# Performance work log

Hardware: AMD Instinct MI355X
Metric: run time of the kernel (lower is better)

The kernel has to match this reference:

```python
import jax, jax.numpy as jnp
import numpy as np

# Model constants (from source: model_dim=1024, head_dim=128, num_heads=8)
L = 8          # num layers (reduced from 16 for tractable reference memory)
T = 2048       # packed tokens, B == 1 (varlen)
DIM = 1024
NH = 8
NKV = 4        # GQA kv heads
HD = 128
KVD = NKV * HD
BLOCK = 128
WS = 3
WIN = WS * BLOCK           # sliding-window size for 'S' layers
ATTN_SCALE = 0.12
PATTERN = 'SSSL'
GATE_CH = 32
EPS = 1.1920929e-07        # torch F.rms_norm default eps = finfo(fp32).eps


def rms_norm(x):
    return x * jax.lax.rsqrt(jnp.mean(x * x, axis=-1, keepdims=True) + EPS)


def apply_rotary(x, cos, sin):
    # x: [T, H, HD]; cos/sin: [T, 1, HD//2]
    d = x.shape[-1] // 2
    x1, x2 = x[..., :d], x[..., d:]
    return jnp.concatenate([x1 * cos + x2 * sin, -x1 * sin + x2 * cos], axis=-1)


def has_ve(layer_idx, n_layer):
    return layer_idx % 2 == (n_layer - 1) % 2


def setup_inputs() -> dict:
    key = jax.random.key(0)
    ks = jax.random.split(key, 9)
    x = jax.random.normal(ks[0], (1, T, DIM), jnp.float32)
    ve = jax.random.normal(ks[1], (L, T, KVD), jnp.float32)
    s = DIM ** -0.5
    Wq = jax.random.normal(ks[2], (L, DIM, NH * HD), jnp.float32) * s
    Wk = jax.random.normal(ks[3], (L, DIM, KVD), jnp.float32) * s
    Wv = jax.random.normal(ks[4], (L, DIM, KVD), jnp.float32) * s
    Wo = jax.random.normal(ks[5], (L, NH * HD, DIM), jnp.float32) * (NH * HD) ** -0.5
    Wgate = jax.random.normal(ks[6], (L, GATE_CH, NKV), jnp.float32) * GATE_CH ** -0.5
    Wfc = jax.random.normal(ks[7], (L, DIM, 4 * DIM), jnp.float32) * s
    Wproj = jax.random.normal(ks[8], (L, 4 * DIM, DIM), jnp.float32) * (4 * DIM) ** -0.5
    # RoPE tables (absolute positions of the packed batch, as in the source)
    inv_freq = 1.0 / (10000.0 ** (jnp.arange(HD // 2, dtype=jnp.float32) / (HD // 2)))
    ang = jnp.arange(T, dtype=jnp.float32)[:, None] * inv_freq[None, :]
    cos = jnp.cos(ang)[:, None, :]
    sin = jnp.sin(ang)[:, None, :]
    # cu_seqlens: 4 packed documents of 512 tokens
    seqlens = jnp.array([0, 512, 1024, 1536, 2048], dtype=jnp.int32)
    return dict(x=x, ve=ve, Wq=Wq, Wk=Wk, Wv=Wv, Wo=Wo, Wgate=Wgate,
                Wfc=Wfc, Wproj=Wproj, cos=cos, sin=sin, seqlens=seqlens)


def reference(x, ve, Wq, Wk, Wv, Wo, Wgate, Wfc, Wproj, cos, sin, seqlens):
    h = x[0]  # [T, DIM], B == 1 (varlen packing)
    pos = jnp.arange(T)
    doc = jnp.searchsorted(seqlens, pos, side='right') - 1
    diff = pos[:, None] - pos[None, :]
    base = (diff >= 0) & (doc[:, None] == doc[None, :])   # causal within doc
    mask_S = base & (diff <= WIN)                         # sliding window
    neg = jnp.float32(-1e30)
    rep = NH // NKV
    for l in range(L):
        xn = rms_norm(h)
        q = (xn @ Wq[l]).reshape(T, NH, HD)
        k = (xn @ Wk[l]).reshape(T, NKV, HD)
        v = (xn @ Wv[l]).reshape(T, NKV, HD)
        if has_ve(l, L):
            gate = 2.0 * jax.nn.sigmoid(xn[:, :GATE_CH] @ Wgate[l])  # [T, NKV]
            v = v + gate[:, :, None] * ve[l].reshape(T, NKV, HD)
        q = rms_norm(apply_rotary(q, cos, sin))
        k = rms_norm(apply_rotary(k, cos, sin))
        k = jnp.repeat(k, rep, axis=1)   # GQA -> full heads
        v2 = jnp.repeat(v, rep, axis=1)
        scores = jnp.einsum('thd,shd->hts', q, k) * ATTN_SCALE  # [NH, T, T]
        mask = mask_S if PATTERN[l % len(PATTERN)] == 'S' else base
        scores = jnp.where(mask[None], scores, neg)
        p = jax.nn.softmax(scores, axis=-1)
        y = jnp.einsum('hts,shd->thd', p, v2).reshape(T, NH * HD)
        h = h + y @ Wo[l]
        m = jnp.square(jax.nn.relu(rms_norm(h) @ Wfc[l]))  # relu(x)^2 MLP
        h = h + m @ Wproj[l]
    return h[None]
```

## Files before the change

kernel.cpp:

```cpp
#include <hip/hip_runtime.h>
#include <hip/hip_bf16.h>
#include <cstdint>
#include <cstddef>

#define TT     2048
#define DMODEL 1024
#define NHQ    8
#define HD     128
#define KVD    512
#define WIN    384
#define EPSF   1.1920929e-07f
#define SCALE  0.12f

typedef __attribute__((ext_vector_type(8))) short bf16x8;
typedef __attribute__((ext_vector_type(4))) float f32x4;

#define WAITV(N)  asm volatile("s_waitcnt vmcnt(" #N ")" ::: "memory")

__device__ __forceinline__ float b2f(unsigned short u) {
    unsigned int i = ((unsigned int)u) << 16; float f; __builtin_memcpy(&f, &i, 4); return f;
}
__device__ __forceinline__ unsigned short f2b(float f) {
    unsigned int i; __builtin_memcpy(&i, &f, 4);
    unsigned int r = (i + 0x7fffu + ((i >> 16) & 1u)) >> 16;
    return (unsigned short)r;
}

__device__ __forceinline__ void gl_lds16(const unsigned short* g, unsigned short* l) {
    __builtin_amdgcn_global_load_lds(
        (const __attribute__((address_space(1))) unsigned int*)g,
        (__attribute__((address_space(3))) unsigned int*)l, 16, 0, 0);
}

__global__ __launch_bounds__(256)
void convT_k(const float* __restrict__ Wq, const float* __restrict__ Wk,
             const float* __restrict__ Wv, const float* __restrict__ Wo,
             const float* __restrict__ Wfc, const float* __restrict__ Wproj,
             unsigned short* __restrict__ Bqkv, unsigned short* __restrict__ Bo,
             unsigned short* __restrict__ Bfc, unsigned short* __restrict__ Bproj)
{
    __shared__ float lt[64][65];
    const int bid = blockIdx.x, tid = threadIdx.x, l = blockIdx.y;

    const float* W; unsigned short* Wt; int K, N, t, nbase;
    if (bid < 256)        { W = Wq    + (size_t)l * 1024 * 1024; Wt = Bqkv  + (size_t)l * 2048 * 1024; K = 1024; N = 1024; t = bid;        nbase = 0;    }
    else if (bid < 384)   { W = Wk    + (size_t)l * 1024 * 512;  Wt = Bqkv  + (size_t)l * 2048 * 1024; K = 1024; N = 512;  t = bid - 256;  nbase = 1024; }
    else if (bid < 512)   { W = Wv    + (size_t)l * 1024 * 512;  Wt = Bqkv  + (size_t)l * 2048 * 1024; K = 1024; N = 512;  t = bid - 384;  nbase = 1536; }
    else if (bid < 768)   { W = Wo    + (size_t)l * 1024 * 1024; Wt = Bo    + (size_t)l * 1024 * 1024; K = 1024; N = 1024; t = bid - 512;  nbase = 0;    }
    else if (bid < 1792)  { W = Wfc   + (size_t)l * 1024 * 4096; Wt = Bfc   + (size_t)l * 4096 * 1024; K = 1024; N = 4096; t = bid - 768;  nbase = 0;    }
    else                  { W = Wproj + (size_t)l * 4096 * 1024; Wt = Bproj + (size_t)l * 1024 * 4096; K = 4096; N = 1024; t = bid - 1792; nbase = 0;    }

    const int ktiles = K >> 6;
    const int k0 = (t % ktiles) * 64, n0 = (t / ktiles) * 64;

    #pragma unroll
    for (int i = 0; i < 4; ++i) {
        int k = (tid >> 4) + i * 16;
        int col4 = (tid & 15) * 4;
        float4 v = *(const float4*)(W + (size_t)(k0 + k) * N + n0 + col4);
        lt[col4 + 0][k] = v.x;
        lt[col4 + 1][k] = v.y;
        lt[col4 + 2][k] = v.z;
        lt[col4 + 3][k] = v.w;
    }
    __syncthreads();
    #pragma unroll
    for (int i = 0; i < 2; ++i) {
        int idx = tid + i * 256;
        int n = idx >> 3, kc = (idx & 7) * 8;
        unsigned short o[8];
        #pragma unroll
        for (int j = 0; j < 8; ++j) o[j] = f2b(lt[n][kc + j]);
        *(uint4*)(Wt + (size_t)(nbase + n0 + n) * K + k0 + kc) = *(const uint4*)o;
    }
}

template<int EPI>
__global__ __launch_bounds__(256, 2)
void gemm4(const unsigned short* __restrict__ A, const unsigned short* __restrict__ Bt,
           unsigned short* __restrict__ Cp, int K, int ksplit, int Ntot)
{
    __shared__ unsigned short As[2 * 128 * 64];
    __shared__ unsigned short Bs[2 * 128 * 64];
    const int BUF = 128 * 64;
    const int tid = threadIdx.x, lane = tid & 63, wv = tid >> 6;

    const int gx = gridDim.x;
    const int nwg = gx * gridDim.y;
    const int ihw = blockIdx.y * gx + blockIdx.x;
    const int q = nwg >> 3, r = nwg & 7;
    const int xcd = ihw & 7, pos = ihw >> 3;
    const int lg = (xcd < r) ? xcd * (q + 1) + pos
                             : r * (q + 1) + (xcd - r) * q + pos;
    const int m0 = (lg % gx) * 128, n0 = (lg / gx) * 128;

    const int kbeg = blockIdx.z * ksplit;
    const int NT = ksplit >> 6;

    const int wr = (wv >> 1) * 64, wc = (wv & 1) * 64;
    const int l15 = lane & 15, g = lane >> 4;
    const int srow = lane >> 3;
    const int sxor = (((lane & 7) ^ srow) << 3);

    const unsigned short* gA0 = A  + (size_t)(m0 + wv * 32 + srow) * K + sxor;
    const unsigned short* gB0 = Bt + (size_t)(n0 + wv * 32 + srow) * K + sxor;

    auto stage = [&](int t) {
        const int b = t & 1;
        const size_t k = (size_t)kbeg + ((size_t)t << 6);
        unsigned short* la = As + b * BUF + (wv * 32) * 64;
        unsigned short* lb = Bs + b * BUF + (wv * 32) * 64;
        #pragma unroll
        for (int c = 0; c < 4; ++c) {
            gl_lds16(gA0 + (size_t)(c * 8) * K + k, la + c * 8 * 64);
            gl_lds16(gB0 + (size_t)(c * 8) * K + k, lb + c * 8 * 64);
        }
    };

    f32x4 acc[4][4] = {};

    stage(0);
    for (int t = 0; t < NT; ++t) {
        if (t + 1 < NT) { stage(t + 1); WAITV(8); }
        else            { WAITV(0); }
        __builtin_amdgcn_s_barrier();

        const unsigned short* Ac = As + (t & 1) * BUF;
        const unsigned short* Bc = Bs + (t & 1) * BUF;
        bf16x8 af[4][2], bfv[4][2];
        #pragma unroll
        for (int mi = 0; mi < 4; ++mi) {
            const int row = wr + mi * 16 + l15, x = row & 7;
            #pragma unroll
            for (int kk = 0; kk < 2; ++kk)
                af[mi][kk] = *(const bf16x8*)(Ac + row * 64 + (((kk * 4 + g) ^ x) << 3));
        }
        #pragma unroll
        for (int ni = 0; ni < 4; ++ni) {
            const int row = wc + ni * 16 + l15, x = row & 7;
            #pragma unroll
            for (int kk = 0; kk < 2; ++kk)
                bfv[ni][kk] = *(const bf16x8*)(Bc + row * 64 + (((kk * 4 + g) ^ x) << 3));
        }
        __builtin_amdgcn_s_setprio(1);
        #pragma unroll
        for (int kk = 0; kk < 2; ++kk)
            #pragma unroll
            for (int mi = 0; mi < 4; ++mi)
                #pragma unroll
                for (int ni = 0; ni < 4; ++ni)
                    acc[mi][ni] = __builtin_amdgcn_mfma_f32_16x16x32_bf16(af[mi][kk], bfv[ni][kk], acc[mi][ni], 0, 0, 0);
        __builtin_amdgcn_s_setprio(0);
        __builtin_amdgcn_s_barrier();
    }

    const int lr4 = (lane >> 4) * 4;
    unsigned short* Cz = Cp + (size_t)blockIdx.z * TT * Ntot;
    #pragma unroll
    for (int mi = 0; mi < 4; ++mi)
        #pragma unroll
        for (int ni = 0; ni < 4; ++ni)
            #pragma unroll
            for (int r2 = 0; r2 < 4; ++r2) {
                int row = m0 + wr + mi * 16 + lr4 + r2;
                int col = n0 + wc + ni * 16 + l15;
                size_t idx = (size_t)row * Ntot + col;
                float v = acc[mi][ni][r2];
                if (EPI == 0) Cz[idx] = f2b(v);
                else {
                    float z = v > 0.f ? v * v : 0.f;
                    Cz[idx] = f2b(z);
                }
            }
}

__global__ __launch_bounds__(256)
void rmsnormF_k(float* __restrict__ h, const unsigned short* __restrict__ part, int nz,
                unsigned short* __restrict__ xn)
{
    const int t = blockIdx.x, tid = threadIdx.x;
    const size_t idx = (size_t)t * (DMODEL / 4) + tid;
    float4 v = ((const float4*)h)[idx];
    for (int z = 0; z < nz; ++z) {
        ushort4 p = ((const ushort4*)part)[idx + (size_t)z * (TT * DMODEL / 4)];
        v.x += b2f(p.x); v.y += b2f(p.y); v.z += b2f(p.z); v.w += b2f(p.w);
    }
    if (nz > 0) ((float4*)h)[idx] = v;

    float ss = v.x*v.x + v.y*v.y + v.z*v.z + v.w*v.w;
    #pragma unroll
    for (int m = 1; m < 64; m <<= 1) ss += __shfl_xor(ss, m);
    __shared__ float red[4];
    if ((tid & 63) == 0) red[tid >> 6] = ss;
    __syncthreads();
    float tot = red[0] + red[1] + red[2] + red[3];
    float rs = rsqrtf(tot * (1.f / DMODEL) + EPSF);
    unsigned short o[4] = { f2b(v.x*rs), f2b(v.y*rs), f2b(v.z*rs), f2b(v.w*rs) };
    *(ushort4*)(xn + (size_t)t * DMODEL + tid * 4) = *(const ushort4*)o;
}

__global__ __launch_bounds__(256)
void reduce_add_k(float* __restrict__ h, const unsigned short* __restrict__ part, int nz)
{
    const int i = blockIdx.x * 256 + threadIdx.x;
    float4 hv = ((float4*)h)[i];
    for (int z = 0; z < nz; ++z) {
        ushort4 p = ((const ushort4*)part)[i + (size_t)z * (TT * DMODEL / 4)];
        hv.x += b2f(p.x); hv.y += b2f(p.y); hv.z += b2f(p.z); hv.w += b2f(p.w);
    }
    ((float4*)h)[i] = hv;
}

__global__ __launch_bounds__(256)
void post_qkv_k(const unsigned short* __restrict__ qkv, const unsigned short* __restrict__ xn,
                const float* __restrict__ cosb, const float* __restrict__ sinb,
                const float* __restrict__ Wgate, const float* __restrict__ vel, int hasve,
                unsigned short* __restrict__ qn, unsigned short* __restrict__ kn,
                unsigned short* __restrict__ vrow)
{
    const size_t S2 = (size_t)TT * 2048;
    const int t = blockIdx.x, tid = threadIdx.x;
    __shared__ float cs[64], sn[64], gate[4];
    if (tid < 64) { cs[tid] = cosb[t * 64 + tid]; sn[tid] = sinb[t * 64 + tid]; }
    if (hasve && tid >= 64 && tid < 68) {
        int g = tid - 64; float a = 0.f;
        for (int c = 0; c < 32; ++c) a += b2f(xn[(size_t)t * DMODEL + c]) * Wgate[c * 4 + g];
        gate[g] = 2.f / (1.f + __expf(-a));
    }
    __syncthreads();
    if (tid < 96) {
        const int hid = tid >> 3, sub = tid & 7;
        const unsigned short* src; unsigned short* dst;
        if (hid < 8) { src = qkv + (size_t)t * 2048 + hid * 128;              dst = qn + (size_t)t * 1024 + hid * 128; }
        else         { src = qkv + (size_t)t * 2048 + 1024 + (hid - 8) * 128; dst = kn + (size_t)t * 512 + (hid - 8) * 128; }
        float o1[8], o2[8], ssum = 0.f;
        #pragma unroll
        for (int j = 0; j < 8; ++j) {
            int jj = sub * 8 + j;
            float x1 = b2f(src[jj])      + b2f(src[jj + S2]);
            float x2 = b2f(src[jj + 64]) + b2f(src[jj + 64 + S2]);
            float c = cs[jj], s = sn[jj];
            o1[j] = x1 * c + x2 * s;
            o2[j] = -x1 * s + x2 * c;
            ssum += o1[j]*o1[j] + o2[j]*o2[j];
        }
        ssum += __shfl_xor(ssum, 1); ssum += __shfl_xor(ssum, 2); ssum += __shfl_xor(ssum, 4);
        float rs = rsqrtf(ssum * (1.f / HD) + EPSF);
        #pragma unroll
        for (int j = 0; j < 8; ++j) {
            int jj = sub * 8 + j;
            dst[jj]      = f2b(o1[j] * rs);
            dst[jj + 64] = f2b(o2[j] * rs);
        }
    }
    {
        int d0 = tid * 2;
        #pragma unroll
        for (int j = 0; j < 2; ++j) {
            int d = d0 + j;
            size_t off = (size_t)t * 2048 + 1536 + d;
            float vv = b2f(qkv[off]) + b2f(qkv[off + S2]);
            if (hasve) vv += gate[d >> 7] * vel[(size_t)t * KVD + d];
            vrow[(size_t)t * KVD + d] = f2b(vv);
        }
    }
}

__global__ __launch_bounds__(256)
void vtrans_k(const unsigned short* __restrict__ vrow, unsigned short* __restrict__ vt)
{
    __shared__ unsigned short lt[64][72];
    const int t0 = blockIdx.x * 64, c0 = blockIdx.y * 64, tid = threadIdx.x;
    #pragma unroll
    for (int i = 0; i < 2; ++i) {
        int r = (tid >> 3) + i * 32;
        int c = (tid & 7) * 8;
        bf16x8 v = *(const bf16x8*)(vrow + (size_t)(t0 + r) * KVD + c0 + c);
        #pragma unroll
        for (int j = 0; j < 8; ++j) lt[c + j][r] = ((unsigned short*)&v)[j];
    }
    __syncthreads();
    #pragma unroll
    for (int i = 0; i < 2; ++i) {
        int r = (tid >> 3) + i * 32;
        int c = (tid & 7) * 8;
        *(bf16x8*)(vt + (size_t)(c0 + r) * TT + t0 + c) = *(const bf16x8*)(&lt[r][c]);
    }
}

__global__ __launch_bounds__(256)
void attn_k(const unsigned short* __restrict__ qn, const unsigned short* __restrict__ kn,
            const unsigned short* __restrict__ vt, unsigned short* __restrict__ y,
            const int* __restrict__ seqlens, int isS)
{
    __shared__ float Ot[4][16][132];
    const int tid = threadIdx.x, w = tid >> 6, lane = tid & 63;
    const int h = blockIdx.y, hkv = h >> 1;
    const int qr = (blockIdx.x * 4 + w) * 16;
    const int s1 = seqlens[1], s2 = seqlens[2], s3 = seqlens[3];
    const int l15 = lane & 15, g = lane >> 4;

    bf16x8 qf[4];
    #pragma unroll
    for (int kk = 0; kk < 4; ++kk)
        qf[kk] = *(const bf16x8*)(qn + (size_t)(qr + l15) * 1024 + h * HD + kk * 32 + g * 8);

    const int row = qr + l15;
    const int drow = (row >= s1) + (row >= s2) + (row >= s3);

    int dq = (qr >= s1) + (qr >= s2) + (qr >= s3);
    int dstart = dq == 0 ? 0 : (dq == 1 ? s1 : (dq == 2 ? s2 : s3));
    int smin = dstart;
    if (isS) { int wlo = qr - WIN; if (wlo > smin) smin = wlo; }
    if (smin < 0) smin = 0;
    const int smax = qr + 16;

    f32x4 acc[8] = {};
    float mrow = -1e30f, lrow = 0.f;

    for (int s0 = smin & ~31; s0 < smax; s0 += 32) {
        f32x4 S[2] = {};
        __builtin_amdgcn_s_setprio(1);
        #pragma unroll
        for (int nb = 0; nb < 2; ++nb) {
            int srow = s0 + nb * 16 + l15;
            #pragma unroll
            for (int kk = 0; kk < 4; ++kk) {
                bf16x8 kf = *(const bf16x8*)(kn + (size_t)srow * KVD + hkv * HD + kk * 32 + g * 8);
                S[nb] = __builtin_amdgcn_mfma_f32_16x16x32_bf16(kf, qf[kk], S[nb], 0, 0, 0);
            }
        }
        __builtin_amdgcn_s_setprio(0);

        float sv[2][4];
        #pragma unroll
        for (int nb = 0; nb < 2; ++nb)
            #pragma unroll
            for (int r = 0; r < 4; ++r) {
                int s = s0 + nb * 16 + 4 * g + r;
                int dcol = (s >= s1) + (s >= s2) + (s >= s3);
                bool valid = (s <= row) && (dcol == drow) && (!isS || (row - s) <= WIN);
                sv[nb][r] = valid ? S[nb][r] * SCALE : -1e30f;
            }

        float pm = sv[0][0];
        #pragma unroll
        for (int r = 1; r < 4; ++r) pm = fmaxf(pm, sv[0][r]);
        #pragma unroll
        for (int r = 0; r < 4; ++r) pm = fmaxf(pm, sv[1][r]);
        pm = fmaxf(pm, __shfl_xor(pm, 16));
        pm = fmaxf(pm, __shfl_xor(pm, 32));
        float mnew = fmaxf(mrow, pm);
        float scl2 = __expf(mrow - mnew);
        float p0[4], p1[4], ps = 0.f;
        #pragma unroll
        for (int r = 0; r < 4; ++r) {
            p0[r] = __expf(sv[0][r] - mnew);
            p1[r] = __expf(sv[1][r] - mnew);
            ps += p0[r] + p1[r];
        }
        ps += __shfl_xor(ps, 16);
        ps += __shfl_xor(ps, 32);
        lrow = lrow * scl2 + ps;
        mrow = mnew;
        #pragma unroll
        for (int nb2 = 0; nb2 < 8; ++nb2) acc[nb2] *= scl2;

        unsigned short pt[8];
        const int base = l15 + ((g & 1) << 5);
        #pragma unroll
        for (int jh = 0; jh < 2; ++jh)
            #pragma unroll
            for (int r = 0; r < 4; ++r) {
                float ta = __shfl(p0[r], base + 16 * jh);
                float tb = __shfl(p1[r], base + 16 * jh);
                pt[jh * 4 + r] = f2b(g >= 2 ? tb : ta);
            }
        bf16x8 pf;
        #pragma unroll
        for (int j = 0; j < 8; ++j) ((unsigned short*)&pf)[j] = pt[j];

        __builtin_amdgcn_s_setprio(1);
        #pragma unroll
        for (int nb2 = 0; nb2 < 8; ++nb2) {
            bf16x8 vf = *(const bf16x8*)(vt + (size_t)(hkv * HD + nb2 * 16 + l15) * TT + s0 + g * 8);
            acc[nb2] = __builtin_amdgcn_mfma_f32_16x16x32_bf16(vf, pf, acc[nb2], 0, 0, 0);
        }
        __builtin_amdgcn_s_setprio(0);
    }

    const float inv = 1.f / lrow;
    #pragma unroll
    for (int nb2 = 0; nb2 < 8; ++nb2)
        #pragma unroll
        for (int r = 0; r < 4; ++r)
            Ot[w][l15][nb2 * 16 + 4 * g + r] = acc[nb2][r] * inv;
    __syncthreads();
    const int qo = lane >> 2, dblk = (lane & 3) * 32;
    #pragma unroll
    for (int i4 = 0; i4 < 4; ++i4) {
        unsigned short ob[8];
        #pragma unroll
        for (int j = 0; j < 8; ++j) ob[j] = f2b(Ot[w][qo][dblk + i4 * 8 + j]);
        *(uint4*)(y + (size_t)(qr + qo) * 1024 + h * HD + dblk + i4 * 8) = *(const uint4*)ob;
    }
}

extern "C" void kernel_launch(void* const* d_in, const int* in_sizes, int n_in,
                              void* d_out, int out_size, void* d_ws, size_t ws_size,
                              hipStream_t stream)
{
    const float* x       = (const float*)d_in[0];
    const float* ve      = (const float*)d_in[1];
    const float* Wq      = (const float*)d_in[2];
    const float* Wk      = (const float*)d_in[3];
    const float* Wv      = (const float*)d_in[4];
    const float* Wo      = (const float*)d_in[5];
    const float* Wgate   = (const float*)d_in[6];
    const float* Wfc     = (const float*)d_in[7];
    const float* Wproj   = (const float*)d_in[8];
    const float* cosb    = (const float*)d_in[9];
    const float* sinb    = (const float*)d_in[10];
    const int*   seqlens = (const int*)d_in[11];

    float* h = (float*)d_out;
    char* ws = (char*)d_ws;
    unsigned short* xn    = (unsigned short*)(ws);
    unsigned short* qn    = (unsigned short*)(ws + (4ull  << 20));
    unsigned short* kn    = (unsigned short*)(ws + (8ull  << 20));
    unsigned short* vrow  = (unsigned short*)(ws + (10ull << 20));
    unsigned short* vt    = (unsigned short*)(ws + (12ull << 20));
    unsigned short* yb    = (unsigned short*)(ws + (14ull << 20));
    unsigned short* mb    = (unsigned short*)(ws + (18ull << 20));
    unsigned short* part  = (unsigned short*)(ws + (34ull << 20));
    unsigned short* Bqkv  = (unsigned short*)(ws + (50ull  << 20));
    unsigned short* Bo    = (unsigned short*)(ws + (82ull  << 20));
    unsigned short* Bfc   = (unsigned short*)(ws + (98ull  << 20));
    unsigned short* Bproj = (unsigned short*)(ws + (162ull << 20));

    hipMemcpyAsync(h, x, (size_t)TT * DMODEL * sizeof(float), hipMemcpyDeviceToDevice, stream);

    convT_k<<<dim3(2816, 8), 256, 0, stream>>>(Wq, Wk, Wv, Wo, Wfc, Wproj,
                                               Bqkv, Bo, Bfc, Bproj);

    for (int l = 0; l < 8; ++l) {
        int hasve = (l % 2) == 1;
        int isS   = (l % 4) != 3;

        rmsnormF_k<<<TT, 256, 0, stream>>>(h, part, l == 0 ? 0 : 4, xn);

        gemm4<0><<<dim3(16, 16, 2), 256, 0, stream>>>(xn, Bqkv + (size_t)l * 2048 * 1024,
                                                      part, 1024, 512, 2048);

        post_qkv_k<<<TT, 256, 0, stream>>>(part, xn, cosb, sinb,
            Wgate + (size_t)l * 128, ve + (size_t)l * TT * KVD, hasve, qn, kn, vrow);

        vtrans_k<<<dim3(32, 8), 256, 0, stream>>>(vrow, vt);

        attn_k<<<dim3(32, 8), 256, 0, stream>>>(qn, kn, vt, yb, seqlens, isS);

        gemm4<0><<<dim3(16, 8, 2), 256, 0, stream>>>(yb, Bo + (size_t)l * 1024 * 1024,
                                                     part, 1024, 512, 1024);

        rmsnormF_k<<<TT, 256, 0, stream>>>(h, part, 2, xn);

        gemm4<2><<<dim3(16, 32, 1), 256, 0, stream>>>(xn, Bfc + (size_t)l * 4096 * 1024,
                                                      mb, 1024, 1024, 4096);

        gemm4<0><<<dim3(16, 8, 4), 256, 0, stream>>>(mb, Bproj + (size_t)l * 1024 * 4096,
                                                     part, 4096, 1024, 1024);
    }

    reduce_add_k<<<2048, 256, 0, stream>>>(h, part, 4);
}
```

Before: 1.404 ms.

## Use 256x128 GEMM tiles with 8 waves and triple-buffered LDS pipeline

Replaces the 128x128, 4-wave GEMM with a 256x128, 8-wave kernel. It uses a 3-stage LDS ring that prefetches two tiles ahead and drops the trailing barrier. Fragment loads are interleaved with the MFMAs to cut register pressure. The Wo projection now uses split-K of 4, so the following rmsnorm reduces 4 partials. The weight transpose kernel moves to 128x128 tiles and converts to bf16 before writing LDS. This raises per-block data reuse and hides more load latency, at the cost of one block per CU and fewer blocks per grid.

```diff
diff --git a/kernel.cpp b/kernel.cpp
--- a/kernel.cpp
+++ b/kernel.cpp
@@ -39,51 +39,48 @@
              unsigned short* __restrict__ Bqkv, unsigned short* __restrict__ Bo,
              unsigned short* __restrict__ Bfc, unsigned short* __restrict__ Bproj)
 {
-    __shared__ float lt[64][65];
+    __shared__ unsigned short lt[128][130];
     const int bid = blockIdx.x, tid = threadIdx.x, l = blockIdx.y;
 
     const float* W; unsigned short* Wt; int K, N, t, nbase;
-    if (bid < 256)        { W = Wq    + (size_t)l * 1024 * 1024; Wt = Bqkv  + (size_t)l * 2048 * 1024; K = 1024; N = 1024; t = bid;        nbase = 0;    }
-    else if (bid < 384)   { W = Wk    + (size_t)l * 1024 * 512;  Wt = Bqkv  + (size_t)l * 2048 * 1024; K = 1024; N = 512;  t = bid - 256;  nbase = 1024; }
-    else if (bid < 512)   { W = Wv    + (size_t)l * 1024 * 512;  Wt = Bqkv  + (size_t)l * 2048 * 1024; K = 1024; N = 512;  t = bid - 384;  nbase = 1536; }
-    else if (bid < 768)   { W = Wo    + (size_t)l * 1024 * 1024; Wt = Bo    + (size_t)l * 1024 * 1024; K = 1024; N = 1024; t = bid - 512;  nbase = 0;    }
-    else if (bid < 1792)  { W = Wfc   + (size_t)l * 1024 * 4096; Wt = Bfc   + (size_t)l * 4096 * 1024; K = 1024; N = 4096; t = bid - 768;  nbase = 0;    }
-    else                  { W = Wproj + (size_t)l * 4096 * 1024; Wt = Bproj + (size_t)l * 1024 * 4096; K = 4096; N = 1024; t = bid - 1792; nbase = 0;    }
-
-    const int ktiles = K >> 6;
-    const int k0 = (t % ktiles) * 64, n0 = (t / ktiles) * 64;
-
-    #pragma unroll
-    for (int i = 0; i < 4; ++i) {
-        int k = (tid >> 4) + i * 16;
-        int col4 = (tid & 15) * 4;
-        float4 v = *(const float4*)(W + (size_t)(k0 + k) * N + n0 + col4);
-        lt[col4 + 0][k] = v.x;
-        lt[col4 + 1][k] = v.y;
-        lt[col4 + 2][k] = v.z;
-        lt[col4 + 3][k] = v.w;
+    if (bid < 64)         { W = Wq    + (size_t)l * 1024 * 1024; Wt = Bqkv  + (size_t)l * 2048 * 1024; K = 1024; N = 1024; t = bid;       nbase = 0;    }
+    else if (bid < 96)    { W = Wk    + (size_t)l * 1024 * 512;  Wt = Bqkv  + (size_t)l * 2048 * 1024; K = 1024; N = 512;  t = bid - 64;  nbase = 1024; }
+    else if (bid < 128)   { W = Wv    + (size_t)l * 1024 * 512;  Wt = Bqkv  + (size_t)l * 2048 * 1024; K = 1024; N = 512;  t = bid - 96;  nbase = 1536; }
+    else if (bid < 192)   { W = Wo    + (size_t)l * 1024 * 1024; Wt = Bo    + (size_t)l * 1024 * 1024; K = 1024; N = 1024; t = bid - 128; nbase = 0;    }
+    else if (bid < 448)   { W = Wfc   + (size_t)l * 1024 * 4096; Wt = Bfc   + (size_t)l * 4096 * 1024; K = 1024; N = 4096; t = bid - 192; nbase = 0;    }
+    else                  { W = Wproj + (size_t)l * 4096 * 1024; Wt = Bproj + (size_t)l * 1024 * 4096; K = 4096; N = 1024; t = bid - 448; nbase = 0;    }
+
+    const int ktiles = K >> 7;
+    const int kt0 = (t % ktiles) * 128, nt0 = (t / ktiles) * 128;
+
+    #pragma unroll
+    for (int i = 0; i < 32; ++i) {
+        int flat = i * 256 + tid;
+        int k = flat >> 6;
+        int n2 = (flat & 63) * 2;
+        float2 rd = *(const float2*)(W + (size_t)(kt0 + k) * N + nt0 + n2);
+        lt[n2 + 0][k] = f2b(rd.x);
+        lt[n2 + 1][k] = f2b(rd.y);
     }
     __syncthreads();
     #pragma unroll
-    for (int i = 0; i < 2; ++i) {
-        int idx = tid + i * 256;
-        int n = idx >> 3, kc = (idx & 7) * 8;
-        unsigned short o[8];
-        #pragma unroll
-        for (int j = 0; j < 8; ++j) o[j] = f2b(lt[n][kc + j]);
-        *(uint4*)(Wt + (size_t)(nbase + n0 + n) * K + k0 + kc) = *(const uint4*)o;
+    for (int i = 0; i < 8; ++i) {
+        int flat = i * 256 + tid;
+        int n = flat >> 4, kc = (flat & 15) * 8;
+        *(uint4*)(Wt + (size_t)(nbase + nt0 + n) * K + kt0 + kc) = *(const uint4*)(&lt[n][kc]);
     }
 }
 
 template<int EPI>
-__global__ __launch_bounds__(256, 2)
-void gemm4(const unsigned short* __restrict__ A, const unsigned short* __restrict__ Bt,
+__global__ __launch_bounds__(512, 1)
+void gemm5(const unsigned short* __restrict__ A, const unsigned short* __restrict__ Bt,
            unsigned short* __restrict__ Cp, int K, int ksplit, int Ntot)
 {
-    __shared__ unsigned short As[2 * 128 * 64];
-    __shared__ unsigned short Bs[2 * 128 * 64];
-    const int BUF = 128 * 64;
+    __shared__ unsigned short As[3 * 256 * 64];
+    __shared__ unsigned short Bs[3 * 128 * 64];
+    const int ABUF = 256 * 64, BBUF = 128 * 64;
     const int tid = threadIdx.x, lane = tid & 63, wv = tid >> 6;
+    const int wm = wv >> 2, wn = wv & 3;
 
     const int gx = gridDim.x;
     const int nwg = gx * gridDim.y;
@@ -92,78 +89,75 @@
     const int xcd = ihw & 7, pos = ihw >> 3;
     const int lg = (xcd < r) ? xcd * (q + 1) + pos
                              : r * (q + 1) + (xcd - r) * q + pos;
-    const int m0 = (lg % gx) * 128, n0 = (lg / gx) * 128;
+    const int m0 = (lg % gx) * 256, n0 = (lg / gx) * 128;
 
     const int kbeg = blockIdx.z * ksplit;
     const int NT = ksplit >> 6;
 
-    const int wr = (wv >> 1) * 64, wc = (wv & 1) * 64;
     const int l15 = lane & 15, g = lane >> 4;
     const int srow = lane >> 3;
     const int sxor = (((lane & 7) ^ srow) << 3);
 
     const unsigned short* gA0 = A  + (size_t)(m0 + wv * 32 + srow) * K + sxor;
-    const unsigned short* gB0 = Bt + (size_t)(n0 + wv * 32 + srow) * K + sxor;
+    const unsigned short* gB0 = Bt + (size_t)(n0 + wv * 16 + srow) * K + sxor;
 
     auto stage = [&](int t) {
-        const int b = t & 1;
+        const int b = t % 3;
         const size_t k = (size_t)kbeg + ((size_t)t << 6);
-        unsigned short* la = As + b * BUF + (wv * 32) * 64;
-        unsigned short* lb = Bs + b * BUF + (wv * 32) * 64;
-        #pragma unroll
-        for (int c = 0; c < 4; ++c) {
+        unsigned short* la = As + b * ABUF + (wv * 32) * 64;
+        unsigned short* lb = Bs + b * BBUF + (wv * 16) * 64;
+        #pragma unroll
+        for (int c = 0; c < 4; ++c)
             gl_lds16(gA0 + (size_t)(c * 8) * K + k, la + c * 8 * 64);
+        #pragma unroll
+        for (int c = 0; c < 2; ++c)
             gl_lds16(gB0 + (size_t)(c * 8) * K + k, lb + c * 8 * 64);
-        }
     };
 
-    f32x4 acc[4][4] = {};
+    f32x4 acc[8][2] = {};
 
     stage(0);
+    if (NT > 1) stage(1);
+
     for (int t = 0; t < NT; ++t) {
-        if (t + 1 < NT) { stage(t + 1); WAITV(8); }
+        if (t + 1 < NT) { WAITV(6); }
         else            { WAITV(0); }
         __builtin_amdgcn_s_barrier();
-
-        const unsigned short* Ac = As + (t & 1) * BUF;
-        const unsigned short* Bc = Bs + (t & 1) * BUF;
-        bf16x8 af[4][2], bfv[4][2];
-        #pragma unroll
-        for (int mi = 0; mi < 4; ++mi) {
-            const int row = wr + mi * 16 + l15, x = row & 7;
-            #pragma unroll
-            for (int kk = 0; kk < 2; ++kk)
-                af[mi][kk] = *(const bf16x8*)(Ac + row * 64 + (((kk * 4 + g) ^ x) << 3));
-        }
-        #pragma unroll
-        for (int ni = 0; ni < 4; ++ni) {
-            const int row = wc + ni * 16 + l15, x = row & 7;
-            #pragma unroll
-            for (int kk = 0; kk < 2; ++kk)
-                bfv[ni][kk] = *(const bf16x8*)(Bc + row * 64 + (((kk * 4 + g) ^ x) << 3));
-        }
+        if (t + 2 < NT) stage(t + 2);
+
+        const unsigned short* Ac = As + (t % 3) * ABUF;
+        const unsigned short* Bc = Bs + (t % 3) * BBUF;
+
         __builtin_amdgcn_s_setprio(1);
         #pragma unroll
-        for (int kk = 0; kk < 2; ++kk)
-            #pragma unroll
-            for (int mi = 0; mi < 4; ++mi)
-                #pragma unroll
-                for (int ni = 0; ni < 4; ++ni)
-                    acc[mi][ni] = __builtin_amdgcn_mfma_f32_16x16x32_bf16(af[mi][kk], bfv[ni][kk], acc[mi][ni], 0, 0, 0);
+        for (int kk = 0; kk < 2; ++kk) {
+            bf16x8 bfv[2];
+            #pragma unroll
+            for (int ni = 0; ni < 2; ++ni) {
+                const int row = wn * 32 + ni * 16 + l15, x = row & 7;
+                bfv[ni] = *(const bf16x8*)(Bc + row * 64 + (((kk * 4 + g) ^ x) << 3));
+            }
+            #pragma unroll
+            for (int mi = 0; mi < 8; ++mi) {
+                const int row = wm * 128 + mi * 16 + l15, x = row & 7;
+                bf16x8 af = *(const bf16x8*)(Ac + row * 64 + (((kk * 4 + g) ^ x) << 3));
+                acc[mi][0] = __builtin_amdgcn_mfma_f32_16x16x32_bf16(af, bfv[0], acc[mi][0], 0, 0, 0);
+                acc[mi][1] = __builtin_amdgcn_mfma_f32_16x16x32_bf16(af, bfv[1], acc[mi][1], 0, 0, 0);
+            }
+        }
         __builtin_amdgcn_s_setprio(0);
-        __builtin_amdgcn_s_barrier();
-    }
-
-    const int lr4 = (lane >> 4) * 4;
+    }
+
+    const int lr4 = g * 4;
     unsigned short* Cz = Cp + (size_t)blockIdx.z * TT * Ntot;
     #pragma unroll
-    for (int mi = 0; mi < 4; ++mi)
-        #pragma unroll
-        for (int ni = 0; ni < 4; ++ni)
+    for (int mi = 0; mi < 8; ++mi)
+        #pragma unroll
+        for (int ni = 0; ni < 2; ++ni)
             #pragma unroll
             for (int r2 = 0; r2 < 4; ++r2) {
-                int row = m0 + wr + mi * 16 + lr4 + r2;
-                int col = n0 + wc + ni * 16 + l15;
+                int row = m0 + wm * 128 + mi * 16 + lr4 + r2;
+                int col = n0 + wn * 32 + ni * 16 + l15;
                 size_t idx = (size_t)row * Ntot + col;
                 float v = acc[mi][ni][r2];
                 if (EPI == 0) Cz[idx] = f2b(v);
@@ -440,8 +434,8 @@
 
     hipMemcpyAsync(h, x, (size_t)TT * DMODEL * sizeof(float), hipMemcpyDeviceToDevice, stream);
 
-    convT_k<<<dim3(2816, 8), 256, 0, stream>>>(Wq, Wk, Wv, Wo, Wfc, Wproj,
-                                               Bqkv, Bo, Bfc, Bproj);
+    convT_k<<<dim3(704, 8), 256, 0, stream>>>(Wq, Wk, Wv, Wo, Wfc, Wproj,
+                                              Bqkv, Bo, Bfc, Bproj);
 
     for (int l = 0; l < 8; ++l) {
         int hasve = (l % 2) == 1;
@@ -449,8 +443,8 @@
 
         rmsnormF_k<<<TT, 256, 0, stream>>>(h, part, l == 0 ? 0 : 4, xn);
 
-        gemm4<0><<<dim3(16, 16, 2), 256, 0, stream>>>(xn, Bqkv + (size_t)l * 2048 * 1024,
-                                                      part, 1024, 512, 2048);
+        gemm5<0><<<dim3(8, 16, 2), 512, 0, stream>>>(xn, Bqkv + (size_t)l * 2048 * 1024,
+                                                     part, 1024, 512, 2048);
 
         post_qkv_k<<<TT, 256, 0, stream>>>(part, xn, cosb, sinb,
             Wgate + (size_t)l * 128, ve + (size_t)l * TT * KVD, hasve, qn, kn, vrow);
@@ -459,16 +453,16 @@
 
         attn_k<<<dim3(32, 8), 256, 0, stream>>>(qn, kn, vt, yb, seqlens, isS);
 
-        gemm4<0><<<dim3(16, 8, 2), 256, 0, stream>>>(yb, Bo + (size_t)l * 1024 * 1024,
-                                                     part, 1024, 512, 1024);
-
-        rmsnormF_k<<<TT, 256, 0, stream>>>(h, part, 2, xn);
-
-        gemm4<2><<<dim3(16, 32, 1), 256, 0, stream>>>(xn, Bfc + (size_t)l * 4096 * 1024,
-                                                      mb, 1024, 1024, 4096);
-
-        gemm4<0><<<dim3(16, 8, 4), 256, 0, stream>>>(mb, Bproj + (size_t)l * 1024 * 4096,
-                                                     part, 4096, 1024, 1024);
+        gemm5<0><<<dim3(8, 8, 4), 512, 0, stream>>>(yb, Bo + (size_t)l * 1024 * 1024,
+                                                    part, 1024, 256, 1024);
+
+        rmsnormF_k<<<TT, 256, 0, stream>>>(h, part, 4, xn);
+
+        gemm5<2><<<dim3(8, 32, 1), 512, 0, stream>>>(xn, Bfc + (size_t)l * 4096 * 1024,
+                                                     mb, 1024, 1024, 4096);
+
+        gemm5<0><<<dim3(8, 8, 4), 512, 0, stream>>>(mb, Bproj + (size_t)l * 1024 * 4096,
+                                                    part, 4096, 1024, 1024);
     }
 
     reduce_add_k<<<2048, 256, 0, stream>>>(h, part, 4);
```

Result: slower. 1.519 ms (+8.1%).
